# Performance work log

Hardware: AMD Instinct MI355X
Metric: run time of the kernel (lower is better)

## Reference

```python
import jax, jax.numpy as jnp
import numpy as np

B, S, D, H = 2, 2048, 1024, 16
HD = D // H  # 64

def _make_freqs():
    # flux-style rotation matrices: [1,1,S,HD//2,2,2]
    theta = 10000.0
    inv = 1.0 / (theta ** (np.arange(0, HD, 2, dtype=np.float32) / HD))  # [HD//2]
    pos = np.arange(S, dtype=np.float32)
    ang = pos[:, None] * inv[None, :]  # [S, HD//2]
    cos, sin = np.cos(ang), np.sin(ang)
    rot = np.stack([np.stack([cos, -sin], -1), np.stack([sin, cos], -1)], -2)  # [S,HD//2,2,2]
    return jnp.asarray(rot[None, None], dtype=jnp.float32)

def setup_inputs() -> dict:
    key = jax.random.key(0)
    ks = jax.random.split(key, 9)
    sc = 1.0 / np.sqrt(D)
    return {
        "x": jax.random.normal(ks[0], (B, S, D), jnp.float32),
        "freqs": _make_freqs(),
        "Wq": jax.random.normal(ks[1], (D, D), jnp.float32) * sc,
        "bq": jax.random.normal(ks[2], (D,), jnp.float32) * 0.01,
        "Wk": jax.random.normal(ks[3], (D, D), jnp.float32) * sc,
        "bk": jax.random.normal(ks[4], (D,), jnp.float32) * 0.01,
        "Wv": jax.random.normal(ks[5], (D, D), jnp.float32) * sc,
        "bv": jax.random.normal(ks[6], (D,), jnp.float32) * 0.01,
        "Wo": jax.random.normal(ks[7], (D, D), jnp.float32) * sc,
        "bo": jax.random.normal(ks[8], (D,), jnp.float32) * 0.01,
    }

def _apply_rope(xq, xk, freqs):
    # xq/xk: [B,H,S,HD]; freqs: [1,1,S,HD//2,2,2]
    def rot(t):
        t_ = t.reshape(*t.shape[:-1], -1, 1, 2)  # [B,H,S,HD//2,1,2]
        out = freqs[..., 0] * t_[..., 0] + freqs[..., 1] * t_[..., 1]  # [B,H,S,HD//2,2]
        return out.reshape(t.shape).astype(t.dtype)
    return rot(xq), rot(xk)

def reference(x, freqs, Wq, bq, Wk, bk, Wv, bv, Wo, bo):
    b, s, _ = x.shape
    # QKV projections (torch Linear: x @ W.T + b)
    q = (x @ Wq.T + bq).reshape(b, s, H, HD).transpose(0, 2, 1, 3)  # [B,H,S,HD]
    k = (x @ Wk.T + bk).reshape(b, s, H, HD).transpose(0, 2, 1, 3)
    v = (x @ Wv.T + bv).reshape(b, s, H, HD).transpose(0, 2, 1, 3)
    q, k = _apply_rope(q, k, freqs)
    # scaled dot product attention, no mask, no dropout
    scale = 1.0 / jnp.sqrt(jnp.asarray(HD, x.dtype))
    scores = jnp.einsum("bhqd,bhkd->bhqk", q, k) * scale
    attn = jax.nn.softmax(scores, axis=-1)
    o = jnp.einsum("bhqk,bhkd->bhqd", attn, v)  # [B,H,S,HD]
    o = o.transpose(0, 2, 1, 3).reshape(b, s, D)
    return o @ Wo.T + bo
```

## Files before the change

### kernel.cpp

```cpp
#include <hip/hip_runtime.h>
#include <cmath>

#define B_ 2
#define S_ 2048
#define D_ 1024
#define H_ 16
#define HD_ 64
#define M_ 4096

typedef __attribute__((ext_vector_type(8))) short short8;
typedef __attribute__((ext_vector_type(4))) short short4v;
typedef __attribute__((ext_vector_type(4))) float f32x4;

__device__ __forceinline__ short f2bf(float x) {
    unsigned u = __builtin_bit_cast(unsigned, x);
    u += 0x7fffu + ((u >> 16) & 1u);
    return (short)(u >> 16);
}

__device__ __forceinline__ void gload_lds16(const short* g, short* l) {
    __builtin_amdgcn_global_load_lds(
        (const __attribute__((address_space(1))) unsigned int*)g,
        (__attribute__((address_space(3))) unsigned int*)l, 16, 0, 0);
}

__global__ __launch_bounds__(256) void cast_all_kernel(
    const float* __restrict__ x,  const float* __restrict__ Wq,
    const float* __restrict__ Wk, const float* __restrict__ Wv,
    const float* __restrict__ Wo,
    short* __restrict__ xb, short* __restrict__ Wqkvb, short* __restrict__ Wob)
{
    const size_t i = (size_t)blockIdx.x * 256 + threadIdx.x;
    const float* src; short* dst; size_t off;
    if (i < 1048576)      { src = x;  dst = xb;              off = i; }
    else if (i < 1310720) { src = Wq; dst = Wqkvb;           off = i - 1048576; }
    else if (i < 1572864) { src = Wk; dst = Wqkvb + 1048576; off = i - 1310720; }
    else if (i < 1835008) { src = Wv; dst = Wqkvb + 2097152; off = i - 1572864; }
    else                  { src = Wo; dst = Wob;             off = i - 1835008; }
    float4 v = ((const float4*)src)[off];
    short4v o = { f2bf(v.x), f2bf(v.y), f2bf(v.z), f2bf(v.w) };
    ((short4v*)dst)[off] = o;
}

template<int MODE, int TM, int TN>
__global__ __launch_bounds__(256) void gemm_chunk(
    const short* __restrict__ A, const short* __restrict__ Bw,
    const float* __restrict__ b0p, const float* __restrict__ b1p, const float* __restrict__ b2p,
    const float* __restrict__ freqs,
    void* __restrict__ out0, void* __restrict__ out1, void* __restrict__ out2)
{
    constexpr int RT = TM / 32, CT = TN / 32;
    __shared__ __align__(16) short As[4*TM*32];
    __shared__ __align__(16) short Bs[4*TN*32];
    const int t = threadIdx.x;
    const int w = t >> 6;
    const int lane = t & 63;
    const int qd = lane >> 4, l = lane & 15;
    const int n0 = blockIdx.x * TN, m0 = blockIdx.y * TM;
    const int wr = (w >> 1) * (TM/2), wc = (w & 1) * (TN/2);
    const int srow = lane >> 2;
    const int scol = (lane & 3) * 8;

    f32x4 acc[RT][CT] = {};

    for (int k0 = 0; k0 < 1024; k0 += 128) {
        __syncthreads();
        #pragma unroll
        for (int sub = 0; sub < 4; ++sub) {
            #pragma unroll
            for (int j = 0; j < TM/64; ++j) {
                const int rr = (j*4 + w) * 16;
                gload_lds16(A + (size_t)(m0 + rr + srow)*1024 + k0 + sub*32 + scol,
                            &As[sub*TM*32 + rr*32]);
            }
            #pragma unroll
            for (int j = 0; j < TN/64; ++j) {
                const int rr = (j*4 + w) * 16;
                gload_lds16(Bw + (size_t)(n0 + rr + srow)*1024 + k0 + sub*32 + scol,
                            &Bs[sub*TN*32 + rr*32]);
            }
        }
        __syncthreads();
        #pragma unroll
        for (int sub = 0; sub < 4; ++sub) {
            short8 af[RT], bf[CT];
            #pragma unroll
            for (int rt = 0; rt < RT; ++rt)
                af[rt] = *(const short8*)&As[sub*TM*32 + (wr + rt*16 + l)*32 + qd*8];
            #pragma unroll
            for (int ct = 0; ct < CT; ++ct)
                bf[ct] = *(const short8*)&Bs[sub*TN*32 + (wc + ct*16 + l)*32 + qd*8];
            #pragma unroll
            for (int rt = 0; rt < RT; ++rt)
                #pragma unroll
                for (int ct = 0; ct < CT; ++ct)
                    acc[rt][ct] = __builtin_amdgcn_mfma_f32_16x16x32_bf16(af[rt], bf[ct], acc[rt][ct], 0, 0, 0);
        }
    }

    if (MODE == 0) {
        float* out = (float*)out0;
        #pragma unroll
        for (int rt = 0; rt < RT; ++rt)
            #pragma unroll
            for (int ct = 0; ct < CT; ++ct) {
                const int n = n0 + wc + ct*16 + l;
                const float bias = b0p[n];
                #pragma unroll
                for (int r = 0; r < 4; ++r) {
                    const int m = m0 + wr + rt*16 + qd*4 + r;
                    out[(size_t)m*1024 + n] = acc[rt][ct][r] + bias;
                }
            }
    } else {
        const int sel = n0 >> 10;
        const int nb = n0 & 1023;
        const float* bias = (sel == 0) ? b0p : (sel == 1) ? b1p : b2p;
        if (sel < 2) {
            short* outg = (short*)((sel == 0) ? out0 : out1);
            #pragma unroll
            for (int rt = 0; rt < RT; ++rt)
                #pragma unroll
                for (int ct = 0; ct < CT; ++ct) {
                    const int d = nb + wc + ct*16 + l;
                    const float bsv = bias[d];
                    const int h = d >> 6, hd = d & 63;
                    #pragma unroll
                    for (int r = 0; r < 4; ++r) {
                        const int m = m0 + wr + rt*16 + qd*4 + r;
                        const int bb = m >> 11, s = m & 2047;
                        float val = acc[rt][ct][r] + bsv;
                        float pv = __shfl_xor(val, 1);
                        const float* f = freqs + (size_t)s*128 + (size_t)(hd >> 1)*4;
                        float o = (d & 1) ? (f[2]*pv + f[3]*val) : (f[0]*val + f[1]*pv);
                        outg[((size_t)(bb*16 + h)*2048 + s)*64 + hd] = f2bf(o);
                    }
                }
        } else {
            short* outv = (short*)out2;
            #pragma unroll
            for (int rt = 0; rt < RT; ++rt)
                #pragma unroll
                for (int ct = 0; ct < CT; ++ct) {
                    const int d = nb + wc + ct*16 + l;
                    const float bsv = bias[d];
                    const int h = d >> 6, hd = d & 63;
                    const int m0r = m0 + wr + rt*16 + qd*4;
                    const int bb = m0r >> 11, s0 = m0r & 2047;
                    short4v pk;
                    #pragma unroll
                    for (int r = 0; r < 4; ++r) pk[r] = f2bf(acc[rt][ct][r] + bsv);
                    *(short4v*)&outv[((size_t)(bb*16 + h)*64 + hd)*2048 + s0] = pk;
                }
        }
    }
}

__global__ __launch_bounds__(256) void attn_mfma(
    const short* __restrict__ qg, const short* __restrict__ kg,
    const short* __restrict__ vtg, short* __restrict__ og)
{
    __shared__ __align__(16) short KP[128*136];
    __shared__ __align__(16) short Vt[64*136];

    const int t = threadIdx.x;
    const int w = t >> 6;
    const int lane = t & 63;
    const int qd = lane >> 4, l = lane & 15;
    const int q0 = blockIdx.x * 128;
    const int bh = blockIdx.y;

    short8 qf[2][2];
    const short* qb = qg + ((size_t)bh*2048 + q0 + w*32)*64;
    #pragma unroll
    for (int rt = 0; rt < 2; ++rt)
        #pragma unroll
        for (int kf = 0; kf < 2; ++kf)
            qf[rt][kf] = *(const short8*)&qb[(rt*16 + l)*64 + kf*32 + qd*8];

    f32x4 oacc[2][4] = {};
    float lsum[2] = {};

    const short* kbase = kg  + (size_t)bh*2048*64;
    const short* vbase = vtg + (size_t)bh*64*2048;
    const float SC = 0.125f * 1.44269504088896340736f;

    for (int kt = 0; kt < 16; ++kt) {
        __syncthreads();
        {
            const short* src = kbase + (size_t)(kt*128 + (t>>1))*64 + (t&1)*32;
            short* dst = &KP[(t>>1)*136 + (t&1)*32];
            *(short8*)(dst+0)  = *(const short8*)(src+0);
            *(short8*)(dst+8)  = *(const short8*)(src+8);
            *(short8*)(dst+16) = *(const short8*)(src+16);
            *(short8*)(dst+24) = *(const short8*)(src+24);
        }
        {
            const short* src = vbase + (size_t)(t>>2)*2048 + kt*128 + (t&3)*32;
            short* dst = &Vt[(t>>2)*136 + (t&3)*32];
            *(short8*)(dst+0)  = *(const short8*)(src+0);
            *(short8*)(dst+8)  = *(const short8*)(src+8);
            *(short8*)(dst+16) = *(const short8*)(src+16);
            *(short8*)(dst+24) = *(const short8*)(src+24);
        }
        __syncthreads();

        f32x4 sacc[2][8] = {};
        #pragma unroll
        for (int ct = 0; ct < 8; ++ct) {
            short8 k0f = *(const short8*)&KP[(ct*16 + l)*136 + qd*8];
            short8 k1f = *(const short8*)&KP[(ct*16 + l)*136 + 32 + qd*8];
            #pragma unroll
            for (int rt = 0; rt < 2; ++rt) {
                sacc[rt][ct] = __builtin_amdgcn_mfma_f32_16x16x32_bf16(k0f, qf[rt][0], sacc[rt][ct], 0, 0, 0);
                sacc[rt][ct] = __builtin_amdgcn_mfma_f32_16x16x32_bf16(k1f, qf[rt][1], sacc[rt][ct], 0, 0, 0);
            }
        }
        __syncthreads();

        #pragma unroll
        for (int rt = 0; rt < 2; ++rt)
            #pragma unroll
            for (int ct = 0; ct < 8; ++ct) {
                short4v pk;
                #pragma unroll
                for (int r = 0; r < 4; ++r) {
                    float p = exp2f(sacc[rt][ct][r] * SC);
                    lsum[rt] += p;
                    pk[r] = f2bf(p);
                }
                *(short4v*)&KP[(w*32 + rt*16 + l)*136 + ct*16 + qd*4] = pk;
            }

        #pragma unroll
        for (int kf = 0; kf < 4; ++kf) {
            short8 pa0 = *(const short8*)&KP[(w*32 +  0 + l)*136 + kf*32 + qd*8];
            short8 pa1 = *(const short8*)&KP[(w*32 + 16 + l)*136 + kf*32 + qd*8];
            #pragma unroll
            for (int ht = 0; ht < 4; ++ht) {
                short8 vb = *(const short8*)&Vt[(ht*16 + l)*136 + kf*32 + qd*8];
                oacc[0][ht] = __builtin_amdgcn_mfma_f32_16x16x32_bf16(pa0, vb, oacc[0][ht], 0, 0, 0);
                oacc[1][ht] = __builtin_amdgcn_mfma_f32_16x16x32_bf16(pa1, vb, oacc[1][ht], 0, 0, 0);
            }
        }
    }

    #pragma unroll
    for (int rt = 0; rt < 2; ++rt) {
        lsum[rt] += __shfl_xor(lsum[rt], 16);
        lsum[rt] += __shfl_xor(lsum[rt], 32);
    }
    float inv[2][4];
    #pragma unroll
    for (int rt = 0; rt < 2; ++rt)
        #pragma unroll
        for (int r = 0; r < 4; ++r)
            inv[rt][r] = 1.0f / __shfl(lsum[rt], qd*4 + r);

    const int bb = bh >> 4, h = bh & 15;
    #pragma unroll
    for (int rt = 0; rt < 2; ++rt)
        #pragma unroll
        for (int ht = 0; ht < 4; ++ht)
            #pragma unroll
            for (int r = 0; r < 4; ++r) {
                const int s = q0 + w*32 + rt*16 + qd*4 + r;
                og[((size_t)bb*2048 + s)*1024 + h*64 + ht*16 + l] =
                    f2bf(oacc[rt][ht][r] * inv[rt][r]);
            }
}

extern "C" void kernel_launch(void* const* d_in, const int* in_sizes, int n_in,
                              void* d_out, int out_size, void* d_ws, size_t ws_size,
                              hipStream_t stream)
{
    const float* x  = (const float*)d_in[0];
    const float* fr = (const float*)d_in[1];
    const float* Wq = (const float*)d_in[2];
    const float* bq = (const float*)d_in[3];
    const float* Wk = (const float*)d_in[4];
    const float* bk = (const float*)d_in[5];
    const float* Wv = (const float*)d_in[6];
    const float* bv = (const float*)d_in[7];
    const float* Wo = (const float*)d_in[8];
    const float* bo = (const float*)d_in[9];
    float* out = (float*)d_out;

    short* ws    = (short*)d_ws;
    short* xb    = ws;
    short* Wqkvb = xb    + 4194304;
    short* Wob   = Wqkvb + 3145728;
    short* qg    = Wob   + 1048576;
    short* kg    = qg    + 4194304;
    short* vtg   = kg    + 4194304;
    short* og    = vtg   + 4194304;

    cast_all_kernel<<<8192, 256, 0, stream>>>(x, Wq, Wk, Wv, Wo, xb, Wqkvb, Wob);
    gemm_chunk<1,128,64><<<dim3(48, 32), 256, 0, stream>>>(xb, Wqkvb, bq, bk, bv, fr, qg, kg, vtg);
    attn_mfma<<<dim3(16, 32), 256, 0, stream>>>(qg, kg, vtg, og);
    gemm_chunk<0,64,64><<<dim3(16, 64), 256, 0, stream>>>(og, Wob, bo, nullptr, nullptr, nullptr,
                                                          out, nullptr, nullptr);
}
```

Baseline: 248.9 us.

## Double-buffer K/V tiles via async global-to-LDS loads with XOR swizzle in attention

The attention kernel now streams 64-key K/V tiles into double-buffered LDS using direct global-to-LDS loads, prefetching the next tile while the current one is computed. It replaces padded LDS rows with an XOR-swizzled layout to avoid bank conflicts, and gives P its own buffer so it no longer reuses the K area. This drops from three barriers per iteration to one. The softmax-to-bf16 conversion uses the packed v_cvt_pk_bf16_f32 instruction. The trade-off is twice as many loop iterations with smaller tiles, and the kernel relies on the swizzled addressing being consistent between writes and reads.

After: 249.8 us. About the same (+0.3%).

```diff
diff --git a/kernel.cpp b/kernel.cpp
--- a/kernel.cpp
+++ b/kernel.cpp
@@ -160,15 +160,20 @@
     const short* __restrict__ qg, const short* __restrict__ kg,
     const short* __restrict__ vtg, short* __restrict__ og)
 {
-    __shared__ __align__(16) short KP[128*136];
-    __shared__ __align__(16) short Vt[64*136];
+    __shared__ __align__(16) short Kb[2][64*64];
+    __shared__ __align__(16) short Vb[2][64*64];
+    __shared__ __align__(16) short Pb[128*64];
 
     const int t = threadIdx.x;
     const int w = t >> 6;
     const int lane = t & 63;
     const int qd = lane >> 4, l = lane & 15;
+    const int l7 = lane & 7;
     const int q0 = blockIdx.x * 128;
     const int bh = blockIdx.y;
+
+    const int rl  = lane >> 3;
+    const int ss8 = ((lane & 7) ^ rl) << 3;
 
     short8 qf[2][2];
     const short* qb = qg + ((size_t)bh*2048 + q0 + w*32)*64;
@@ -185,64 +190,67 @@
     const short* vbase = vtg + (size_t)bh*64*2048;
     const float SC = 0.125f * 1.44269504088896340736f;
 
-    for (int kt = 0; kt < 16; ++kt) {
-        __syncthreads();
-        {
-            const short* src = kbase + (size_t)(kt*128 + (t>>1))*64 + (t&1)*32;
-            short* dst = &KP[(t>>1)*136 + (t&1)*32];
-            *(short8*)(dst+0)  = *(const short8*)(src+0);
-            *(short8*)(dst+8)  = *(const short8*)(src+8);
-            *(short8*)(dst+16) = *(const short8*)(src+16);
-            *(short8*)(dst+24) = *(const short8*)(src+24);
-        }
-        {
-            const short* src = vbase + (size_t)(t>>2)*2048 + kt*128 + (t&3)*32;
-            short* dst = &Vt[(t>>2)*136 + (t&3)*32];
-            *(short8*)(dst+0)  = *(const short8*)(src+0);
-            *(short8*)(dst+8)  = *(const short8*)(src+8);
-            *(short8*)(dst+16) = *(const short8*)(src+16);
-            *(short8*)(dst+24) = *(const short8*)(src+24);
-        }
-        __syncthreads();
-
-        f32x4 sacc[2][8] = {};
-        #pragma unroll
-        for (int ct = 0; ct < 8; ++ct) {
-            short8 k0f = *(const short8*)&KP[(ct*16 + l)*136 + qd*8];
-            short8 k1f = *(const short8*)&KP[(ct*16 + l)*136 + 32 + qd*8];
+    {
+        gload_lds16(kbase + (size_t)(w*8 + rl)*64 + ss8,        &Kb[0][(w*8)*64]);
+        gload_lds16(kbase + (size_t)(32 + w*8 + rl)*64 + ss8,   &Kb[0][(32 + w*8)*64]);
+        gload_lds16(vbase + (size_t)(w*8 + rl)*2048 + ss8,      &Vb[0][(w*8)*64]);
+        gload_lds16(vbase + (size_t)(32 + w*8 + rl)*2048 + ss8, &Vb[0][(32 + w*8)*64]);
+    }
+    __syncthreads();
+
+    for (int kt = 0; kt < 32; ++kt) {
+        const int buf = kt & 1;
+
+        if (kt + 1 < 32) {
+            const short* k2 = kbase + (size_t)(kt + 1)*64*64;
+            const short* v2 = vbase + (size_t)(kt + 1)*64;
+            gload_lds16(k2 + (size_t)(w*8 + rl)*64 + ss8,        &Kb[buf^1][(w*8)*64]);
+            gload_lds16(k2 + (size_t)(32 + w*8 + rl)*64 + ss8,   &Kb[buf^1][(32 + w*8)*64]);
+            gload_lds16(v2 + (size_t)(w*8 + rl)*2048 + ss8,      &Vb[buf^1][(w*8)*64]);
+            gload_lds16(v2 + (size_t)(32 + w*8 + rl)*2048 + ss8, &Vb[buf^1][(32 + w*8)*64]);
+        }
+
+        f32x4 sacc[2][4] = {};
+        #pragma unroll
+        for (int ct = 0; ct < 4; ++ct) {
+            short8 k0f = *(const short8*)&Kb[buf][(ct*16 + l)*64 + (((0 + qd) ^ l7) << 3)];
+            short8 k1f = *(const short8*)&Kb[buf][(ct*16 + l)*64 + (((4 + qd) ^ l7) << 3)];
             #pragma unroll
             for (int rt = 0; rt < 2; ++rt) {
                 sacc[rt][ct] = __builtin_amdgcn_mfma_f32_16x16x32_bf16(k0f, qf[rt][0], sacc[rt][ct], 0, 0, 0);
                 sacc[rt][ct] = __builtin_amdgcn_mfma_f32_16x16x32_bf16(k1f, qf[rt][1], sacc[rt][ct], 0, 0, 0);
             }
         }
-        __syncthreads();
 
         #pragma unroll
         for (int rt = 0; rt < 2; ++rt)
             #pragma unroll
-            for (int ct = 0; ct < 8; ++ct) {
-                short4v pk;
-                #pragma unroll
-                for (int r = 0; r < 4; ++r) {
-                    float p = exp2f(sacc[rt][ct][r] * SC);
-                    lsum[rt] += p;
-                    pk[r] = f2bf(p);
-                }
-                *(short4v*)&KP[(w*32 + rt*16 + l)*136 + ct*16 + qd*4] = pk;
-            }
-
-        #pragma unroll
-        for (int kf = 0; kf < 4; ++kf) {
-            short8 pa0 = *(const short8*)&KP[(w*32 +  0 + l)*136 + kf*32 + qd*8];
-            short8 pa1 = *(const short8*)&KP[(w*32 + 16 + l)*136 + kf*32 + qd*8];
+            for (int ct = 0; ct < 4; ++ct) {
+                float p0 = exp2f(sacc[rt][ct][0] * SC);
+                float p1 = exp2f(sacc[rt][ct][1] * SC);
+                float p2 = exp2f(sacc[rt][ct][2] * SC);
+                float p3 = exp2f(sacc[rt][ct][3] * SC);
+                lsum[rt] += (p0 + p1) + (p2 + p3);
+                union { unsigned u[2]; short4v s; } cv;
+                asm("v_cvt_pk_bf16_f32 %0, %1, %2" : "=v"(cv.u[0]) : "v"(p0), "v"(p1));
+                asm("v_cvt_pk_bf16_f32 %0, %1, %2" : "=v"(cv.u[1]) : "v"(p2), "v"(p3));
+                *(short4v*)&Pb[(w*32 + rt*16 + l)*64 + (((ct*32 + qd*8) ^ (l7 << 4)) >> 1)] = cv.s;
+            }
+
+        #pragma unroll
+        for (int kf = 0; kf < 2; ++kf) {
+            const int so = ((kf*4 + qd) ^ l7) << 3;
+            short8 pa0 = *(const short8*)&Pb[(w*32 +  0 + l)*64 + so];
+            short8 pa1 = *(const short8*)&Pb[(w*32 + 16 + l)*64 + so];
             #pragma unroll
             for (int ht = 0; ht < 4; ++ht) {
-                short8 vb = *(const short8*)&Vt[(ht*16 + l)*136 + kf*32 + qd*8];
+                short8 vb = *(const short8*)&Vb[buf][(ht*16 + l)*64 + so];
                 oacc[0][ht] = __builtin_amdgcn_mfma_f32_16x16x32_bf16(pa0, vb, oacc[0][ht], 0, 0, 0);
                 oacc[1][ht] = __builtin_amdgcn_mfma_f32_16x16x32_bf16(pa1, vb, oacc[1][ht], 0, 0, 0);
             }
         }
+
+        __syncthreads();
     }
 
     #pragma unroll
```
